# Kernel tuning notes

Measured on AMD Instinct MI355X. Metric: run time of the kernel, lower is better.

Reference implementation:

```python
import jax, jax.numpy as jnp
import numpy as np

K, Q, DIM = 64, 128, 1024
TF_W, DE_W, FFT_W = 1.0, 0.8, 0.6  # opt.TF_weight / DE_weight / FFT_weight


def setup_inputs() -> dict:
    key = jax.random.key(0)
    ks = jax.random.split(key, 9)
    def feats(k):
        return jax.random.normal(k, (K, Q, DIM), dtype=jnp.float32)
    def protos(k):
        return jax.random.normal(k, (K, DIM), dtype=jnp.float32)
    def var(k):
        # positive variances, bounded away from zero
        return jax.random.uniform(k, (K,), dtype=jnp.float32) + 0.5
    return {
        "TFq_output": feats(ks[0]), "TFs_proto": protos(ks[1]), "TF_variance": var(ks[2]),
        "DEq_output": feats(ks[3]), "DEs_proto": protos(ks[4]), "DE_variance": var(ks[5]),
        "FFTq_output": feats(ks[6]), "FFTs_proto": protos(ks[7]), "FFT_variance": var(ks[8]),
    }


def _mah_dist(xq, proto, variance):
    # ||x - p||^2 / var via expansion: avoids materializing (num, protonum, dim)
    x2 = jnp.sum(xq * xq, axis=1, keepdims=True)            # (num, 1)
    p2 = jnp.sum(proto * proto, axis=1)[None, :]            # (1, protonum)
    xp = xq @ proto.T                                       # (num, protonum)
    return (x2 - 2.0 * xp + p2) / variance[None, :]


def _modality(xq, proto, variance, w):
    logits = -_mah_dist(xq, proto, variance)
    pred = w * jax.nn.softmax(logits, axis=1)
    mahloss = -(w * jax.nn.log_softmax(logits, axis=1))
    return pred, mahloss


def reference(TFq_output, TFs_proto, TF_variance,
              DEq_output, DEs_proto, DE_variance,
              FFTq_output, FFTs_proto, FFT_variance):
    k, q, _ = TFq_output.shape
    y = jnp.repeat(jnp.arange(k), q)                         # (k*q,)

    tf_pred, tf_loss = _modality(TFq_output.reshape(k * q, -1), TFs_proto, TF_variance, TF_W)
    de_pred, de_loss = _modality(DEq_output.reshape(k * q, -1), DEs_proto, DE_variance, DE_W)
    fft_pred, fft_loss = _modality(FFTq_output.reshape(k * q, -1), FFTs_proto, FFT_variance, FFT_W)

    fusion_loss = tf_loss + de_loss + fft_loss               # (k*q, k)
    loss = jnp.take_along_axis(fusion_loss, y[:, None], axis=1).squeeze(-1).mean()

    pred_mah = tf_pred + de_pred + fft_pred
    pred = jnp.argmax(pred_mah, axis=1)
    acc = (pred == y).astype(jnp.float32).mean()
    return (loss, acc)
```

## Files before the change

kernel.cpp:

```cpp
#include <hip/hip_runtime.h>


typedef _Float16 half8 __attribute__((ext_vector_type(8)));
typedef float    floatx4 __attribute__((ext_vector_type(4)));

#define NCLS   64
#define QPC    128
#define DIM    1024
#define NROWS  (NCLS * QPC)
#define NRT    (NROWS / 16)

#define OFF_W      0
#define W_BYTES    (3 * NCLS * DIM * 2)
#define OFF_P2     W_BYTES
#define OFF_LP     (OFF_P2 + 3 * NCLS * 4)
#define OFF_CP     (OFF_LP + NRT * 4)
#define WS_NEED    (OFF_CP + NRT * 4)

__global__ __launch_bounds__(64) void prep_protos(
    const float* __restrict__ Ptf, const float* __restrict__ Pde,
    const float* __restrict__ Pff, _Float16* __restrict__ W,
    float* __restrict__ p2)
{
    const int m    = blockIdx.x >> 5;
    const int kcg  = blockIdx.x & 31;
    const int lane = threadIdx.x;
    const int l15  = lane & 15;
    const int quad = lane >> 4;
    const float* __restrict__ P = (m == 0) ? Ptf : (m == 1) ? Pde : Pff;

    #pragma unroll
    for (int t = 0; t < 4; ++t) {
        const float* src = P + (size_t)(t * 16 + l15) * DIM + kcg * 32 + quad * 8;
        const float4 b0 = *reinterpret_cast<const float4*>(src);
        const float4 b1 = *reinterpret_cast<const float4*>(src + 4);
        half8 h;
        h[0] = (_Float16)b0.x; h[1] = (_Float16)b0.y;
        h[2] = (_Float16)b0.z; h[3] = (_Float16)b0.w;
        h[4] = (_Float16)b1.x; h[5] = (_Float16)b1.y;
        h[6] = (_Float16)b1.z; h[7] = (_Float16)b1.w;
        *reinterpret_cast<half8*>(W + ((size_t)(m * 32 + kcg) * 4 + t) * 512 + lane * 8) = h;

        float s = b0.x*b0.x + b0.y*b0.y + b0.z*b0.z + b0.w*b0.w
                + b1.x*b1.x + b1.y*b1.y + b1.z*b1.z + b1.w*b1.w;
        s += __shfl_xor(s, 16);
        s += __shfl_xor(s, 32);
        if (quad == 0) atomicAdd(&p2[m * 64 + t * 16 + l15], s);
    }
}

__global__ __launch_bounds__(768, 6) void fusion_all(
    const float* __restrict__ Xtf, const float* __restrict__ Xde,
    const float* __restrict__ Xff,
    const float* __restrict__ Vtf, const float* __restrict__ Vde,
    const float* __restrict__ Vff,
    const _Float16* __restrict__ W, const float* __restrict__ p2g,
    float* __restrict__ lossPart,
    float* __restrict__ cntPart)
{
    __shared__ float x2s[3][16];
    __shared__ float mxW[3][4][16];
    __shared__ float sW[3][4][16];
    __shared__ float predS[3][16][66];
    __shared__ float lossW[12];
    __shared__ float cntW[4];

    const int tid  = threadIdx.x;
    const int w    = tid >> 6;
    const int lane = tid & 63;
    const int l15  = lane & 15;
    const int quad = lane >> 4;
    const int m    = w >> 2;
    const int cq   = w & 3;
    const int rowBase = blockIdx.x * 16;

    const float* __restrict__ X = (m == 0) ? Xtf : (m == 1) ? Xde : Xff;
    const float* __restrict__ V = (m == 0) ? Vtf : (m == 1) ? Vde : Vff;
    const float  wgt = (m == 0) ? 1.0f : (m == 1) ? 0.8f : 0.6f;

    const float* __restrict__ xr = X + (size_t)(rowBase + l15) * DIM + quad * 8;
    const _Float16* __restrict__ wb = W + ((size_t)(m * 32) * 4 + cq) * 512 + lane * 8;

    floatx4 d = (floatx4){0.f, 0.f, 0.f, 0.f};
    float x2p = 0.0f;

    #pragma unroll 2
    for (int kc = 0; kc < 32; ++kc) {
        const float4 a0 = *reinterpret_cast<const float4*>(xr + kc * 32);
        const float4 a1 = *reinterpret_cast<const float4*>(xr + kc * 32 + 4);
        const half8 bf = *reinterpret_cast<const half8*>(wb + (size_t)kc * 2048);

        if (cq == 0)
            x2p += a0.x*a0.x + a0.y*a0.y + a0.z*a0.z + a0.w*a0.w
                 + a1.x*a1.x + a1.y*a1.y + a1.z*a1.z + a1.w*a1.w;

        half8 af;
        af[0] = (_Float16)a0.x; af[1] = (_Float16)a0.y;
        af[2] = (_Float16)a0.z; af[3] = (_Float16)a0.w;
        af[4] = (_Float16)a1.x; af[5] = (_Float16)a1.y;
        af[6] = (_Float16)a1.z; af[7] = (_Float16)a1.w;

        d = __builtin_amdgcn_mfma_f32_16x16x32_f16(af, bf, d, 0, 0, 0);
    }

    if (cq == 0) {
        x2p += __shfl_xor(x2p, 16);
        x2p += __shfl_xor(x2p, 32);
        if (quad == 0) x2s[m][l15] = x2p;
    }
    __syncthreads();

    const int col = cq * 16 + l15;
    const float vc  = V[col];
    const float p2c = p2g[m * 64 + col];
    float lg[4];
    #pragma unroll
    for (int r = 0; r < 4; ++r)
        lg[r] = (2.0f * d[r] - x2s[m][quad * 4 + r] - p2c) / vc;

    #pragma unroll
    for (int r = 0; r < 4; ++r) {
        float mx = lg[r];
        #pragma unroll
        for (int dl = 1; dl <= 8; dl <<= 1) mx = fmaxf(mx, __shfl_xor(mx, dl));
        if (l15 == 0) mxW[m][cq][quad * 4 + r] = mx;
    }
    __syncthreads();

    float gmx[4];
    #pragma unroll
    for (int r = 0; r < 4; ++r) {
        const int row = quad * 4 + r;
        gmx[r] = fmaxf(fmaxf(mxW[m][0][row], mxW[m][1][row]),
                       fmaxf(mxW[m][2][row], mxW[m][3][row]));
        float s = expf(lg[r] - gmx[r]);
        #pragma unroll
        for (int dl = 1; dl <= 8; dl <<= 1) s += __shfl_xor(s, dl);
        if (l15 == 0) sW[m][cq][quad * 4 + r] = s;
    }
    __syncthreads();

    const int y = rowBase >> 7;
    float lossAcc = 0.0f;
    #pragma unroll
    for (int r = 0; r < 4; ++r) {
        const int row = quad * 4 + r;
        const float lse = gmx[r] + logf(sW[m][0][row] + sW[m][1][row]
                                      + sW[m][2][row] + sW[m][3][row]);
        if (col == y) lossAcc += wgt * (lse - lg[r]);
        predS[m][row][col] = wgt * expf(lg[r] - lse);
    }
    #pragma unroll
    for (int dl = 1; dl <= 32; dl <<= 1) lossAcc += __shfl_xor(lossAcc, dl);
    if (lane == 0) lossW[w] = lossAcc;
    __syncthreads();

    if (w < 4) {
        float cnt = 0.0f;
        #pragma unroll
        for (int r4 = 0; r4 < 4; ++r4) {
            const int row = w * 4 + r4;
            float bv = predS[0][row][lane] + predS[1][row][lane]
                     + predS[2][row][lane];
            int bc = lane;
            #pragma unroll
            for (int dl = 1; dl <= 32; dl <<= 1) {
                const float ov = __shfl_xor(bv, dl);
                const int   oc = __shfl_xor(bc, dl);
                if (ov > bv || (ov == bv && oc < bc)) { bv = ov; bc = oc; }
            }
            if (bc == y) cnt += 1.0f;
        }
        if (lane == 0) cntW[w] = cnt;
    }
    __syncthreads();

    if (tid == 0) {
        float L = 0.0f;
        #pragma unroll
        for (int i = 0; i < 12; ++i) L += lossW[i];
        lossPart[blockIdx.x] = L;
        cntPart[blockIdx.x]  = cntW[0] + cntW[1] + cntW[2] + cntW[3];
    }
}

__global__ __launch_bounds__(256) void finalize2(
    const float* __restrict__ lossPart, const float* __restrict__ cntPart,
    float* __restrict__ out)
{
    const int tid  = threadIdx.x;
    const int lane = tid & 63;
    const int v    = tid >> 6;
    float l = 0.0f, c = 0.0f;
    for (int i = tid; i < NRT; i += 256) l += lossPart[i];
    for (int i = tid; i < NRT; i += 256) c += cntPart[i];
    #pragma unroll
    for (int dl = 1; dl <= 32; dl <<= 1) {
        l += __shfl_xor(l, dl);
        c += __shfl_xor(c, dl);
    }
    __shared__ float sl[4], sc[4];
    if (lane == 0) { sl[v] = l; sc[v] = c; }
    __syncthreads();
    if (tid == 0) {
        out[0] = (sl[0] + sl[1] + sl[2] + sl[3]) * (1.0f / NROWS);
        out[1] = (sc[0] + sc[1] + sc[2] + sc[3]) * (1.0f / NROWS);
    }
}

#define NWAVES 12
#define KSPLIT 4
#define KSLICE (DIM / KSPLIT)
#define NITER  (KSLICE / 32)
#define DSTRIDE 17
#define PSTRIDE 65

__global__ __launch_bounds__(NWAVES * 64) void fusion_loss_fallback(
    const float* __restrict__ Xtf, const float* __restrict__ Ptf, const float* __restrict__ Vtf,
    const float* __restrict__ Xde, const float* __restrict__ Pde, const float* __restrict__ Vde,
    const float* __restrict__ Xff, const float* __restrict__ Pff, const float* __restrict__ Vff,
    float* __restrict__ out)
{
    __shared__ float dpart[NWAVES][64 * DSTRIDE];
    __shared__ float x2part[NWAVES][16];
    __shared__ float p2part[NWAVES][64];
    __shared__ float predL[16 * PSTRIDE];
    __shared__ float lossL;

    const int tid  = threadIdx.x;
    const int wave = tid >> 6;
    const int lane = tid & 63;
    const int l15  = lane & 15;
    const int quad = lane >> 4;
    const int m    = wave >> 2;
    const int kq   = wave & 3;
    const int rowBase = blockIdx.x * 16;

    for (int i = tid; i < 16 * PSTRIDE; i += NWAVES * 64) predL[i] = 0.0f;
    if (tid == 0) lossL = 0.0f;

    const float* __restrict__ X = (m == 0) ? Xtf : (m == 1) ? Xde : Xff;
    const float* __restrict__ P = (m == 0) ? Ptf : (m == 1) ? Pde : Pff;
    const float* __restrict__ V = (m == 0) ? Vtf : (m == 1) ? Vde : Vff;
    const float  w = (m == 0) ? 1.0f : (m == 1) ? 0.8f : 0.6f;

    floatx4 d[4];
    #pragma unroll
    for (int t = 0; t < 4; ++t) d[t] = (floatx4){0.f, 0.f, 0.f, 0.f};
    float x2p    = 0.0f;
    float p2p[4] = {0.f, 0.f, 0.f, 0.f};

    const float* xrow = X + (size_t)(rowBase + l15) * DIM + kq * KSLICE + quad * 8;
    const float* prow[4];
    #pragma unroll
    for (int t = 0; t < 4; ++t)
        prow[t] = P + (size_t)(t * 16 + l15) * DIM + kq * KSLICE + quad * 8;

    #pragma unroll 2
    for (int kc = 0; kc < NITER; ++kc) {
        const int ko = kc * 32;
        const float4 a0 = *reinterpret_cast<const float4*>(xrow + ko);
        const float4 a1 = *reinterpret_cast<const float4*>(xrow + ko + 4);
        float4 b0[4], b1[4];
        #pragma unroll
        for (int t = 0; t < 4; ++t) {
            b0[t] = *reinterpret_cast<const float4*>(prow[t] + ko);
            b1[t] = *reinterpret_cast<const float4*>(prow[t] + ko + 4);
        }
        x2p += a0.x*a0.x + a0.y*a0.y + a0.z*a0.z + a0.w*a0.w
             + a1.x*a1.x + a1.y*a1.y + a1.z*a1.z + a1.w*a1.w;
        half8 af;
        af[0] = (_Float16)a0.x; af[1] = (_Float16)a0.y;
        af[2] = (_Float16)a0.z; af[3] = (_Float16)a0.w;
        af[4] = (_Float16)a1.x; af[5] = (_Float16)a1.y;
        af[6] = (_Float16)a1.z; af[7] = (_Float16)a1.w;
        #pragma unroll
        for (int t = 0; t < 4; ++t) {
            p2p[t] += b0[t].x*b0[t].x + b0[t].y*b0[t].y + b0[t].z*b0[t].z + b0[t].w*b0[t].w
                    + b1[t].x*b1[t].x + b1[t].y*b1[t].y + b1[t].z*b1[t].z + b1[t].w*b1[t].w;
            half8 bf;
            bf[0] = (_Float16)b0[t].x; bf[1] = (_Float16)b0[t].y;
            bf[2] = (_Float16)b0[t].z; bf[3] = (_Float16)b0[t].w;
            bf[4] = (_Float16)b1[t].x; bf[5] = (_Float16)b1[t].y;
            bf[6] = (_Float16)b1[t].z; bf[7] = (_Float16)b1[t].w;
            d[t] = __builtin_amdgcn_mfma_f32_16x16x32_f16(af, bf, d[t], 0, 0, 0);
        }
    }

    x2p += __shfl_xor(x2p, 16);
    x2p += __shfl_xor(x2p, 32);
    #pragma unroll
    for (int t = 0; t < 4; ++t) {
        p2p[t] += __shfl_xor(p2p[t], 16);
        p2p[t] += __shfl_xor(p2p[t], 32);
    }
    {
        float* dp = &dpart[wave][lane * DSTRIDE];
        #pragma unroll
        for (int t = 0; t < 4; ++t)
            *reinterpret_cast<float4*>(dp + t * 4) =
                make_float4(d[t][0], d[t][1], d[t][2], d[t][3]);
        if (quad == 0) {
            x2part[wave][l15] = x2p;
            #pragma unroll
            for (int t = 0; t < 4; ++t) p2part[wave][t * 16 + l15] = p2p[t];
        }
    }
    __syncthreads();

    const int y = rowBase >> 7;

    if (kq == 0) {
        floatx4 dsum[4];
        #pragma unroll
        for (int t = 0; t < 4; ++t) dsum[t] = (floatx4){0.f, 0.f, 0.f, 0.f};
        float x2r[4] = {0.f, 0.f, 0.f, 0.f};
        float p2c[4] = {0.f, 0.f, 0.f, 0.f};
        #pragma unroll
        for (int k2 = 0; k2 < KSPLIT; ++k2) {
            const int wv = m * 4 + k2;
            const float* src = &dpart[wv][lane * DSTRIDE];
            #pragma unroll
            for (int t = 0; t < 4; ++t) {
                const float4 vv = *reinterpret_cast<const float4*>(src + t * 4);
                dsum[t][0] += vv.x; dsum[t][1] += vv.y; dsum[t][2] += vv.z; dsum[t][3] += vv.w;
            }
            #pragma unroll
            for (int r = 0; r < 4; ++r) x2r[r] += x2part[wv][quad * 4 + r];
            #pragma unroll
            for (int t = 0; t < 4; ++t) p2c[t] += p2part[wv][t * 16 + l15];
        }
        float vc[4];
        #pragma unroll
        for (int t = 0; t < 4; ++t) vc[t] = V[t * 16 + l15];

        float lossAcc = 0.0f;
        #pragma unroll
        for (int r = 0; r < 4; ++r) {
            float lg[4];
            #pragma unroll
            for (int t = 0; t < 4; ++t)
                lg[t] = (2.0f * dsum[t][r] - x2r[r] - p2c[t]) / vc[t];
            float mx = fmaxf(fmaxf(lg[0], lg[1]), fmaxf(lg[2], lg[3]));
            #pragma unroll
            for (int dl = 1; dl <= 8; dl <<= 1) mx = fmaxf(mx, __shfl_xor(mx, dl));
            float s = expf(lg[0] - mx) + expf(lg[1] - mx)
                    + expf(lg[2] - mx) + expf(lg[3] - mx);
            #pragma unroll
            for (int dl = 1; dl <= 8; dl <<= 1) s += __shfl_xor(s, dl);
            const float lse = mx + logf(s);
            const int row = quad * 4 + r;
            #pragma unroll
            for (int t = 0; t < 4; ++t) {
                const int colc = t * 16 + l15;
                if (colc == y) lossAcc += w * (lse - lg[t]);
                atomicAdd(&predL[row * PSTRIDE + colc], w * expf(lg[t] - lse));
            }
        }
        #pragma unroll
        for (int dl = 1; dl <= 32; dl <<= 1) lossAcc += __shfl_xor(lossAcc, dl);
        if (lane == 0) atomicAdd(&lossL, lossAcc);
    }
    __syncthreads();

    if (wave == 0) {
        float cnt = 0.0f;
        #pragma unroll 1
        for (int r = 0; r < 16; ++r) {
            float bv = predL[r * PSTRIDE + lane];
            int   bc = lane;
            #pragma unroll
            for (int dl = 1; dl <= 32; dl <<= 1) {
                const float ov = __shfl_xor(bv, dl);
                const int   oc = __shfl_xor(bc, dl);
                if (ov > bv || (ov == bv && oc < bc)) { bv = ov; bc = oc; }
            }
            if (lane == 0 && bc == y) cnt += 1.0f;
        }
        if (lane == 0) {
            atomicAdd(&out[0], lossL * (1.0f / NROWS));
            atomicAdd(&out[1], cnt * (1.0f / NROWS));
        }
    }
}

extern "C" void kernel_launch(void* const* d_in, const int* in_sizes, int n_in,
                              void* d_out, int out_size, void* d_ws, size_t ws_size,
                              hipStream_t stream) {
    const float* Xtf = (const float*)d_in[0];
    const float* Ptf = (const float*)d_in[1];
    const float* Vtf = (const float*)d_in[2];
    const float* Xde = (const float*)d_in[3];
    const float* Pde = (const float*)d_in[4];
    const float* Vde = (const float*)d_in[5];
    const float* Xff = (const float*)d_in[6];
    const float* Pff = (const float*)d_in[7];
    const float* Vff = (const float*)d_in[8];
    float* out = (float*)d_out;

    if (ws_size >= (size_t)WS_NEED) {
        char* ws = (char*)d_ws;
        _Float16* W     = (_Float16*)(ws + OFF_W);
        float*    p2    = (float*)(ws + OFF_P2);
        float*    lossP = (float*)(ws + OFF_LP);
        float*    cntP  = (float*)(ws + OFF_CP);

        hipMemsetAsync(p2, 0, 3 * NCLS * sizeof(float), stream);
        prep_protos<<<dim3(96), dim3(64), 0, stream>>>(Ptf, Pde, Pff, W, p2);
        fusion_all<<<dim3(NRT), dim3(768), 0, stream>>>(
            Xtf, Xde, Xff, Vtf, Vde, Vff, W, p2, lossP, cntP);
        finalize2<<<dim3(1), dim3(256), 0, stream>>>(lossP, cntP, out);
    } else {
        hipMemsetAsync(out, 0, 2 * sizeof(float), stream);
        fusion_loss_fallback<<<dim3(NROWS / 16), dim3(NWAVES * 64), 0, stream>>>(
            Xtf, Ptf, Vtf, Xde, Pde, Vde, Xff, Pff, Vff, out);
    }
}
```

Measured before the change: 176.6 us.

## Stage query rows into LDS via async global_load_lds double buffering

Replaces the direct per-lane global loads of X with cooperative 16-byte global-to-LDS DMA transfers into a double-buffered, XOR-swizzled shared tile. All four column-quarter waves of a modality previously reloaded the same X rows from global memory; each row is now fetched once and read from LDS by every wave. This adds 48KB of LDS per block, which can lower occupancy against the 768x6 launch bound, and adds a __syncthreads per chunk.

New measurement: 146.8 us. -16.9%, faster.

```diff
diff --git a/kernel.cpp b/kernel.cpp
--- a/kernel.cpp
+++ b/kernel.cpp
@@ -16,6 +16,13 @@
 #define OFF_LP     (OFF_P2 + 3 * NCLS * 4)
 #define OFF_CP     (OFF_LP + NRT * 4)
 #define WS_NEED    (OFF_CP + NRT * 4)
+
+__device__ __forceinline__ void dma16(const float* g, float* l) {
+    __builtin_amdgcn_global_load_lds(
+        (const __attribute__((address_space(1))) void*)g,
+        (__attribute__((address_space(3))) void*)l,
+        16, 0, 0);
+}
 
 __global__ __launch_bounds__(64) void prep_protos(
     const float* __restrict__ Ptf, const float* __restrict__ Pde,
@@ -58,6 +65,7 @@
     float* __restrict__ lossPart,
     float* __restrict__ cntPart)
 {
+    __shared__ float buf[2][3][16][128];
     __shared__ float x2s[3][16];
     __shared__ float mxW[3][4][16];
     __shared__ float sW[3][4][16];
@@ -78,29 +86,56 @@
     const float* __restrict__ V = (m == 0) ? Vtf : (m == 1) ? Vde : Vff;
     const float  wgt = (m == 0) ? 1.0f : (m == 1) ? 0.8f : 0.6f;
 
-    const float* __restrict__ xr = X + (size_t)(rowBase + l15) * DIM + quad * 8;
+    const int rl0 = cq * 4 + (lane >> 5);
+    const int rl1 = rl0 + 2;
+    const int sc0 = ((lane & 31) * 4) ^ ((rl0 & 7) * 4);
+    const int sc1 = ((lane & 31) * 4) ^ ((rl1 & 7) * 4);
+    const float* __restrict__ s0 = X + (size_t)(rowBase + rl0) * DIM + sc0;
+    const float* __restrict__ s1 = X + (size_t)(rowBase + rl1) * DIM + sc1;
+
     const _Float16* __restrict__ wb = W + ((size_t)(m * 32) * 4 + cq) * 512 + lane * 8;
 
     floatx4 d = (floatx4){0.f, 0.f, 0.f, 0.f};
     float x2p = 0.0f;
 
-    #pragma unroll 2
-    for (int kc = 0; kc < 32; ++kc) {
-        const float4 a0 = *reinterpret_cast<const float4*>(xr + kc * 32);
-        const float4 a1 = *reinterpret_cast<const float4*>(xr + kc * 32 + 4);
-        const half8 bf = *reinterpret_cast<const half8*>(wb + (size_t)kc * 2048);
-
-        if (cq == 0)
-            x2p += a0.x*a0.x + a0.y*a0.y + a0.z*a0.z + a0.w*a0.w
-                 + a1.x*a1.x + a1.y*a1.y + a1.z*a1.z + a1.w*a1.w;
-
-        half8 af;
-        af[0] = (_Float16)a0.x; af[1] = (_Float16)a0.y;
-        af[2] = (_Float16)a0.z; af[3] = (_Float16)a0.w;
-        af[4] = (_Float16)a1.x; af[5] = (_Float16)a1.y;
-        af[6] = (_Float16)a1.z; af[7] = (_Float16)a1.w;
-
-        d = __builtin_amdgcn_mfma_f32_16x16x32_f16(af, bf, d, 0, 0, 0);
+    const int sw     = (l15 & 7) << 2;
+    const int rowOff = l15 * 128;
+
+    dma16(s0, &buf[0][m][cq * 4][0]);
+    dma16(s1, &buf[0][m][cq * 4 + 2][0]);
+    __syncthreads();
+
+    #pragma unroll
+    for (int c = 0; c < 8; ++c) {
+        if (c < 7) {
+            dma16(s0 + (c + 1) * 128, &buf[(c + 1) & 1][m][cq * 4][0]);
+            dma16(s1 + (c + 1) * 128, &buf[(c + 1) & 1][m][cq * 4 + 2][0]);
+        }
+        asm volatile("" ::: "memory");
+
+        const float* tb = &buf[c & 1][m][0][0];
+        #pragma unroll
+        for (int kc = 0; kc < 4; ++kc) {
+            const float4 a0 = *reinterpret_cast<const float4*>(
+                tb + rowOff + kc * 32 + ((quad * 8) ^ sw));
+            const float4 a1 = *reinterpret_cast<const float4*>(
+                tb + rowOff + kc * 32 + (((quad * 8) + 4) ^ sw));
+            const half8 bf = *reinterpret_cast<const half8*>(
+                wb + (size_t)(c * 4 + kc) * 2048);
+
+            if (cq == 0)
+                x2p += a0.x*a0.x + a0.y*a0.y + a0.z*a0.z + a0.w*a0.w
+                     + a1.x*a1.x + a1.y*a1.y + a1.z*a1.z + a1.w*a1.w;
+
+            half8 af;
+            af[0] = (_Float16)a0.x; af[1] = (_Float16)a0.y;
+            af[2] = (_Float16)a0.z; af[3] = (_Float16)a0.w;
+            af[4] = (_Float16)a1.x; af[5] = (_Float16)a1.y;
+            af[6] = (_Float16)a1.z; af[7] = (_Float16)a1.w;
+
+            d = __builtin_amdgcn_mfma_f32_16x16x32_f16(af, bf, d, 0, 0, 0);
+        }
+        __syncthreads();
     }
 
     if (cq == 0) {
```

## Split K across wave pairs, each wave computing all 64 columns with software pipelining

Applied to the files above, without the earlier changes.

Work is now split differently. Before, 12 waves each computed one 16-column slice over the full K. Now 6 waves per block each cover half of K for all 64 columns, so the activation row tile is loaded and converted once per modality rather than four times. Loads are software-pipelined three stages deep, and the two K-halves are combined through shared memory. Softmax is then done in-register by one wave per modality, which removes two barrier rounds. The costs are more registers per wave (16 accumulators plus staged buffers) and fewer waves in total for latency hiding.

After: 151.9 us. -14.0%, faster.

```diff
diff --git a/kernel.cpp b/kernel.cpp
--- a/kernel.cpp
+++ b/kernel.cpp
@@ -49,7 +49,7 @@
     }
 }
 
-__global__ __launch_bounds__(768, 6) void fusion_all(
+__global__ __launch_bounds__(384, 3) void fusion_all(
     const float* __restrict__ Xtf, const float* __restrict__ Xde,
     const float* __restrict__ Xff,
     const float* __restrict__ Vtf, const float* __restrict__ Vde,
@@ -58,11 +58,10 @@
     float* __restrict__ lossPart,
     float* __restrict__ cntPart)
 {
+    __shared__ float cmb[3][17][64];
     __shared__ float x2s[3][16];
-    __shared__ float mxW[3][4][16];
-    __shared__ float sW[3][4][16];
     __shared__ float predS[3][16][66];
-    __shared__ float lossW[12];
+    __shared__ float lossW[6];
     __shared__ float cntW[4];
 
     const int tid  = threadIdx.x;
@@ -70,89 +69,137 @@
     const int lane = tid & 63;
     const int l15  = lane & 15;
     const int quad = lane >> 4;
-    const int m    = w >> 2;
-    const int cq   = w & 3;
+    const int m    = w >> 1;
+    const int h    = w & 1;
     const int rowBase = blockIdx.x * 16;
 
     const float* __restrict__ X = (m == 0) ? Xtf : (m == 1) ? Xde : Xff;
     const float* __restrict__ V = (m == 0) ? Vtf : (m == 1) ? Vde : Vff;
     const float  wgt = (m == 0) ? 1.0f : (m == 1) ? 0.8f : 0.6f;
 
-    const float* __restrict__ xr = X + (size_t)(rowBase + l15) * DIM + quad * 8;
-    const _Float16* __restrict__ wb = W + ((size_t)(m * 32) * 4 + cq) * 512 + lane * 8;
-
-    floatx4 d = (floatx4){0.f, 0.f, 0.f, 0.f};
+    const float* __restrict__ xr =
+        X + (size_t)(rowBase + l15) * DIM + h * 512 + quad * 8;
+    const _Float16* __restrict__ wb =
+        W + ((size_t)(m * 32 + h * 16) * 4) * 512 + lane * 8;
+
+    floatx4 dd[4];
+    #pragma unroll
+    for (int n = 0; n < 4; ++n) dd[n] = (floatx4){0.f, 0.f, 0.f, 0.f};
     float x2p = 0.0f;
 
-    #pragma unroll 2
-    for (int kc = 0; kc < 32; ++kc) {
-        const float4 a0 = *reinterpret_cast<const float4*>(xr + kc * 32);
-        const float4 a1 = *reinterpret_cast<const float4*>(xr + kc * 32 + 4);
-        const half8 bf = *reinterpret_cast<const half8*>(wb + (size_t)kc * 2048);
-
-        if (cq == 0)
-            x2p += a0.x*a0.x + a0.y*a0.y + a0.z*a0.z + a0.w*a0.w
-                 + a1.x*a1.x + a1.y*a1.y + a1.z*a1.z + a1.w*a1.w;
-
-        half8 af;
-        af[0] = (_Float16)a0.x; af[1] = (_Float16)a0.y;
-        af[2] = (_Float16)a0.z; af[3] = (_Float16)a0.w;
-        af[4] = (_Float16)a1.x; af[5] = (_Float16)a1.y;
-        af[6] = (_Float16)a1.z; af[7] = (_Float16)a1.w;
-
-        d = __builtin_amdgcn_mfma_f32_16x16x32_f16(af, bf, d, 0, 0, 0);
-    }
-
-    if (cq == 0) {
-        x2p += __shfl_xor(x2p, 16);
-        x2p += __shfl_xor(x2p, 32);
+    float4 aA[4], aB[4];
+    half8  bf[4][4];
+
+#define FENCE asm volatile("" ::: "memory")
+
+#define ISSUE(S, KC) do {                                                   \
+    aA[S] = *reinterpret_cast<const float4*>(xr + (KC) * 32);               \
+    aB[S] = *reinterpret_cast<const float4*>(xr + (KC) * 32 + 4);           \
+    bf[S][0] = *reinterpret_cast<const half8*>(wb + ((KC)*4 + 0) * 512);    \
+    bf[S][1] = *reinterpret_cast<const half8*>(wb + ((KC)*4 + 1) * 512);    \
+    bf[S][2] = *reinterpret_cast<const half8*>(wb + ((KC)*4 + 2) * 512);    \
+    bf[S][3] = *reinterpret_cast<const half8*>(wb + ((KC)*4 + 3) * 512);    \
+} while (0)
+
+#define CONSUME(S) do {                                                     \
+    const float4 A0 = aA[S];                                                \
+    const float4 A1 = aB[S];                                                \
+    x2p += A0.x*A0.x + A0.y*A0.y + A0.z*A0.z + A0.w*A0.w                    \
+         + A1.x*A1.x + A1.y*A1.y + A1.z*A1.z + A1.w*A1.w;                   \
+    half8 af;                                                               \
+    af[0] = (_Float16)A0.x; af[1] = (_Float16)A0.y;                         \
+    af[2] = (_Float16)A0.z; af[3] = (_Float16)A0.w;                         \
+    af[4] = (_Float16)A1.x; af[5] = (_Float16)A1.y;                         \
+    af[6] = (_Float16)A1.z; af[7] = (_Float16)A1.w;                         \
+    dd[0] = __builtin_amdgcn_mfma_f32_16x16x32_f16(af, bf[S][0], dd[0],0,0,0); \
+    dd[1] = __builtin_amdgcn_mfma_f32_16x16x32_f16(af, bf[S][1], dd[1],0,0,0); \
+    dd[2] = __builtin_amdgcn_mfma_f32_16x16x32_f16(af, bf[S][2], dd[2],0,0,0); \
+    dd[3] = __builtin_amdgcn_mfma_f32_16x16x32_f16(af, bf[S][3], dd[3],0,0,0); \
+} while (0)
+
+#define STEP(J) do {                                                        \
+    if ((J) + 3 < 16) { ISSUE(((J) + 3) & 3, (J) + 3); }                    \
+    FENCE;                                                                  \
+    CONSUME((J) & 3);                                                       \
+} while (0)
+
+    ISSUE(0, 0); FENCE;
+    ISSUE(1, 1); FENCE;
+    ISSUE(2, 2); FENCE;
+
+    STEP(0);  STEP(1);  STEP(2);  STEP(3);
+    STEP(4);  STEP(5);  STEP(6);  STEP(7);
+    STEP(8);  STEP(9);  STEP(10); STEP(11);
+    STEP(12); STEP(13); STEP(14); STEP(15);
+
+#undef STEP
+#undef CONSUME
+#undef ISSUE
+#undef FENCE
+
+    x2p += __shfl_xor(x2p, 16);
+    x2p += __shfl_xor(x2p, 32);
+
+    if (h == 1) {
+        #pragma unroll
+        for (int n = 0; n < 4; ++n)
+            #pragma unroll
+            for (int r = 0; r < 4; ++r)
+                cmb[m][n * 4 + r][lane] = dd[n][r];
+        cmb[m][16][lane] = x2p;
+    }
+    __syncthreads();
+    if (h == 0) {
+        #pragma unroll
+        for (int n = 0; n < 4; ++n)
+            #pragma unroll
+            for (int r = 0; r < 4; ++r)
+                dd[n][r] += cmb[m][n * 4 + r][lane];
+        x2p += cmb[m][16][lane];
         if (quad == 0) x2s[m][l15] = x2p;
-    }
-    __syncthreads();
-
-    const int col = cq * 16 + l15;
-    const float vc  = V[col];
-    const float p2c = p2g[m * 64 + col];
-    float lg[4];
-    #pragma unroll
-    for (int r = 0; r < 4; ++r)
-        lg[r] = (2.0f * d[r] - x2s[m][quad * 4 + r] - p2c) / vc;
-
-    #pragma unroll
-    for (int r = 0; r < 4; ++r) {
-        float mx = lg[r];
-        #pragma unroll
-        for (int dl = 1; dl <= 8; dl <<= 1) mx = fmaxf(mx, __shfl_xor(mx, dl));
-        if (l15 == 0) mxW[m][cq][quad * 4 + r] = mx;
-    }
-    __syncthreads();
-
-    float gmx[4];
-    #pragma unroll
-    for (int r = 0; r < 4; ++r) {
-        const int row = quad * 4 + r;
-        gmx[r] = fmaxf(fmaxf(mxW[m][0][row], mxW[m][1][row]),
-                       fmaxf(mxW[m][2][row], mxW[m][3][row]));
-        float s = expf(lg[r] - gmx[r]);
-        #pragma unroll
-        for (int dl = 1; dl <= 8; dl <<= 1) s += __shfl_xor(s, dl);
-        if (l15 == 0) sW[m][cq][quad * 4 + r] = s;
     }
     __syncthreads();
 
     const int y = rowBase >> 7;
     float lossAcc = 0.0f;
-    #pragma unroll
-    for (int r = 0; r < 4; ++r) {
-        const int row = quad * 4 + r;
-        const float lse = gmx[r] + logf(sW[m][0][row] + sW[m][1][row]
-                                      + sW[m][2][row] + sW[m][3][row]);
-        if (col == y) lossAcc += wgt * (lse - lg[r]);
-        predS[m][row][col] = wgt * expf(lg[r] - lse);
+    if (h == 0) {
+        float vc[4], p2c[4];
+        #pragma unroll
+        for (int n = 0; n < 4; ++n) {
+            const int col = n * 16 + l15;
+            vc[n]  = V[col];
+            p2c[n] = p2g[m * 64 + col];
+        }
+        #pragma unroll
+        for (int r = 0; r < 4; ++r) {
+            const int row  = quad * 4 + r;
+            const float x2r = x2s[m][row];
+            float lg[4];
+            float mx = -3.4e38f;
+            #pragma unroll
+            for (int n = 0; n < 4; ++n) {
+                lg[n] = (2.0f * dd[n][r] - x2r - p2c[n]) / vc[n];
+                mx = fmaxf(mx, lg[n]);
+            }
+            #pragma unroll
+            for (int dl = 1; dl <= 8; dl <<= 1) mx = fmaxf(mx, __shfl_xor(mx, dl));
+            float s = 0.0f;
+            #pragma unroll
+            for (int n = 0; n < 4; ++n) s += expf(lg[n] - mx);
+            #pragma unroll
+            for (int dl = 1; dl <= 8; dl <<= 1) s += __shfl_xor(s, dl);
+            const float lse = mx + logf(s);
+            #pragma unroll
+            for (int n = 0; n < 4; ++n) {
+                const int col = n * 16 + l15;
+                if (col == y) lossAcc += wgt * (lse - lg[n]);
+                predS[m][row][col] = wgt * expf(lg[n] - lse);
+            }
+        }
     }
     #pragma unroll
     for (int dl = 1; dl <= 32; dl <<= 1) lossAcc += __shfl_xor(lossAcc, dl);
-    if (lane == 0) lossW[w] = lossAcc;
+    if (lane == 0) lossW[w] = (h == 0) ? lossAcc : 0.0f;
     __syncthreads();
 
     if (w < 4) {
@@ -178,7 +225,7 @@
     if (tid == 0) {
         float L = 0.0f;
         #pragma unroll
-        for (int i = 0; i < 12; ++i) L += lossW[i];
+        for (int i = 0; i < 6; ++i) L += lossW[i];
         lossPart[blockIdx.x] = L;
         cntPart[blockIdx.x]  = cntW[0] + cntW[1] + cntW[2] + cntW[3];
     }
@@ -407,7 +454,7 @@
 
         hipMemsetAsync(p2, 0, 3 * NCLS * sizeof(float), stream);
         prep_protos<<<dim3(96), dim3(64), 0, stream>>>(Ptf, Pde, Pff, W, p2);
-        fusion_all<<<dim3(NRT), dim3(768), 0, stream>>>(
+        fusion_all<<<dim3(NRT), dim3(384), 0, stream>>>(
             Xtf, Xde, Xff, Vtf, Vde, Vff, W, p2, lossP, cntP);
         finalize2<<<dim3(1), dim3(256), 0, stream>>>(lossP, cntP, out);
     } else {
```
